# Kernel optimization log

Measured on AMD Instinct MI355X. Metric: run time of the kernel, lower is better.

Reference implementation:

```python
import jax, jax.numpy as jnp
import numpy as np

N_NODES = 100000
N_EDGES = 3200000
D_IN = 128
D_HID = 128
D_FF = 256
N_CLASSES = 26
N_GRAPHS = 512


def setup_inputs() -> dict:
    key = jax.random.key(0)
    ks = jax.random.split(key, 12)
    s = 0.05
    return {
        "x": jax.random.normal(ks[0], (N_NODES, D_IN), dtype=jnp.float32),
        "edge_index": jax.random.randint(ks[1], (2, N_EDGES), 0, N_NODES, dtype=jnp.int64),
        "batch": jnp.sort(jax.random.randint(ks[2], (N_NODES,), 0, N_GRAPHS, dtype=jnp.int64)),
        "W1": jax.random.normal(ks[3], (D_IN, D_HID), dtype=jnp.float32) * s,
        "b1": jnp.zeros((D_HID,), dtype=jnp.float32),
        "W2": jax.random.normal(ks[4], (D_HID, D_HID), dtype=jnp.float32) * s,
        "b2": jnp.zeros((D_HID,), dtype=jnp.float32),
        "W3": jax.random.normal(ks[5], (D_HID, D_HID), dtype=jnp.float32) * s,
        "b3": jnp.zeros((D_HID,), dtype=jnp.float32),
        "Wfc": jax.random.normal(ks[6], (D_HID, D_FF), dtype=jnp.float32) * s,
        "bfc": jnp.zeros((D_FF,), dtype=jnp.float32),
        "Wfc2": jax.random.normal(ks[7], (D_FF, N_CLASSES), dtype=jnp.float32) * s,
        "bfc2": jnp.zeros((N_CLASSES,), dtype=jnp.float32),
    }


def _gcn_layer(x, src, dst, norm, W, b):
    # GCNConv: h = x @ W; out[dst] += norm_e * h[src]; out += b
    h = x @ W                                   # [N, D]
    msg = h[src] * norm[:, None]                # [E+N, D] gather + scale
    agg = jax.ops.segment_sum(msg, dst, num_segments=N_NODES)
    return agg + b


def reference(x, edge_index, batch, W1, b1, W2, b2, W3, b3, Wfc, bfc, Wfc2, bfc2):
    # add self-loops (PyG GCNConv default) and compute symmetric normalization once
    loop = jnp.arange(N_NODES, dtype=edge_index.dtype)
    src = jnp.concatenate([edge_index[0], loop])
    dst = jnp.concatenate([edge_index[1], loop])
    deg = jax.ops.segment_sum(jnp.ones_like(dst, dtype=x.dtype), dst, num_segments=N_NODES)
    dinv = jnp.where(deg > 0, jax.lax.rsqrt(deg), 0.0)
    norm = dinv[src] * dinv[dst]               # D^{-1/2} A_hat D^{-1/2}

    h = jax.nn.relu(_gcn_layer(x, src, dst, norm, W1, b1))
    h = jax.nn.relu(_gcn_layer(h, src, dst, norm, W2, b2))
    h = jax.nn.relu(_gcn_layer(h, src, dst, norm, W3, b3))

    # global mean pool over graphs
    sums = jax.ops.segment_sum(h, batch, num_segments=N_GRAPHS)       # [G, D]
    cnts = jax.ops.segment_sum(jnp.ones((h.shape[0],), h.dtype), batch, num_segments=N_GRAPHS)
    pooled = sums / jnp.maximum(cnts, 1.0)[:, None]

    out = jax.nn.relu(pooled @ Wfc + bfc)       # dropout is identity at inference
    return out @ Wfc2 + bfc2                    # [G, num_classes]
```

## Files before the change

### kernel.cpp

```cpp
#include <hip/hip_runtime.h>
#include <hip/hip_bf16.h>

typedef __bf16 bf16;
typedef __attribute__((ext_vector_type(8))) __bf16 bf16x8;
typedef __attribute__((ext_vector_type(4))) float f32x4;

constexpr int N_NODES   = 100000;
constexpr int N_PAD     = 100032;
constexpr int D         = 128;
constexpr int D_FF      = 256;
constexpr int N_CLASSES = 26;
constexpr int N_GRAPHS  = 512;
constexpr int NB1       = 256;
constexpr int NBUCK     = (N_NODES + 511) / 512;

__device__ inline float2 bf2f(unsigned u) {
    float lo = __uint_as_float(u << 16);
    float hi = __uint_as_float(u & 0xffff0000u);
    return make_float2(lo, hi);
}


__global__ __launch_bounds__(1024) void p1_hist(const int* __restrict__ edst,
                                                int* __restrict__ gcount, int e) {
    __shared__ int cnt[NBUCK];
    for (int t = threadIdx.x; t < NBUCK; t += 1024) cnt[t] = 0;
    __syncthreads();
    int chunk = (e + NB1 - 1) / NB1;
    int lo = blockIdx.x * chunk;
    int hi = min(e, lo + chunk);
    for (int i = lo + threadIdx.x; i < hi; i += 1024)
        atomicAdd(&cnt[edst[i] >> 9], 1);
    __syncthreads();
    for (int t = threadIdx.x; t < NBUCK; t += 1024)
        gcount[t * NB1 + blockIdx.x] = cnt[t];
}

__global__ __launch_bounds__(256) void scan1(const int* __restrict__ in,
                                             int* out, int* bsum, int n) {
    __shared__ int sd[256];
    int i = blockIdx.x * 256 + threadIdx.x;
    int v = (i < n) ? in[i] : 0;
    sd[threadIdx.x] = v; __syncthreads();
    for (int off = 1; off < 256; off <<= 1) {
        int t = (threadIdx.x >= off) ? sd[threadIdx.x - off] : 0;
        __syncthreads();
        sd[threadIdx.x] += t;
        __syncthreads();
    }
    if (i < n) out[i] = sd[threadIdx.x] - v;
    if (threadIdx.x == 255) bsum[blockIdx.x] = sd[255];
}

__global__ __launch_bounds__(1024) void misc_kernel(const int* __restrict__ bsum,
                                                    int* __restrict__ boff, int nb,
                                                    const int* __restrict__ batch,
                                                    int* __restrict__ starts, int n,
                                                    const float* __restrict__ W0,
                                                    const float* __restrict__ W1,
                                                    const float* __restrict__ W2,
                                                    bf16* __restrict__ WT3) {
    int t = threadIdx.x;
    if (blockIdx.x == 0) {
        if (t <= N_GRAPHS) {
            int lo = 0, hi = n;
            while (lo < hi) {
                int mid = (lo + hi) >> 1;
                if (batch[mid] < t) lo = mid + 1; else hi = mid;
            }
            starts[t] = lo;
        }
        __shared__ int sd[1024];
        int v = (t < nb) ? bsum[t] : 0;
        sd[t] = v; __syncthreads();
        for (int off = 1; off < 1024; off <<= 1) {
            int x = (t >= off) ? sd[t - off] : 0;
            __syncthreads();
            sd[t] += x;
            __syncthreads();
        }
        if (t < nb) boff[t] = sd[t] - v;
    } else {
        int idx = (blockIdx.x - 1) * 1024 + t;
        int l = idx >> 14;
        int rem = idx & 16383;
        int nn = rem >> 7;
        int kk = rem & 127;
        const float* W = (l == 0) ? W0 : (l == 1) ? W1 : W2;
        WT3[idx] = (bf16)W[kk * D + nn];
    }
}

__global__ __launch_bounds__(1024) void p3_scatter(const int* __restrict__ esrc,
                                                   const int* __restrict__ edst,
                                                   const int* __restrict__ gbase,
                                                   const int* __restrict__ boff,
                                                   int* __restrict__ ebuf, int e) {
    __shared__ int cur[NBUCK];
    for (int t = threadIdx.x; t < NBUCK; t += 1024)
        cur[t] = gbase[t * NB1 + blockIdx.x] + boff[t];
    __syncthreads();
    int chunk = (e + NB1 - 1) / NB1;
    int lo = blockIdx.x * chunk;
    int hi = min(e, lo + chunk);
    for (int i = lo + threadIdx.x; i < hi; i += 1024) {
        int d = edst[i], s = esrc[i];
        int pos = atomicAdd(&cur[d >> 9], 1);
        ebuf[pos] = (s << 9) | (d & 511);
    }
}

__global__ __launch_bounds__(1024) void p45_fill(const int* __restrict__ ebuf,
                                                 const int* __restrict__ gbase,
                                                 const int* __restrict__ boff,
                                                 float* __restrict__ dinv,
                                                 int* __restrict__ rowptr,
                                                 int* __restrict__ csrc, int e, int n) {
    __shared__ int cnt[512];
    __shared__ int ps[512];
    __shared__ int cur[512];
    int b = blockIdx.x, t = threadIdx.x;
    if (t < 512) cnt[t] = 0;
    __syncthreads();
    int lo = gbase[b * NB1] + boff[b];
    int hi = (b + 1 < NBUCK) ? gbase[(b + 1) * NB1] + boff[b + 1] : e;
    for (int i = lo + t; i < hi; i += 1024)
        atomicAdd(&cnt[ebuf[i] & 511], 1);
    __syncthreads();
    int a = (t < 512) ? cnt[t] : 0;
    if (t < 512) ps[t] = a;
    __syncthreads();
    for (int off = 1; off < 512; off <<= 1) {
        int v = (t >= off && t < 512) ? ps[t - off] : 0;
        __syncthreads();
        if (t < 512) ps[t] += v;
        __syncthreads();
    }
    if (t < 512) {
        int g0 = lo + ps[t] - a;
        int node = b * 512 + t;
        cur[t] = g0;
        if (node < n) {
            rowptr[node] = g0;
            dinv[node] = 1.0f / sqrtf((float)(a + 1));
        }
    }
    if (b == 0 && t == 0) rowptr[n] = e;
    __syncthreads();
    for (int i = lo + t; i < hi; i += 1024) {
        int pe = ebuf[i];
        int pos = atomicAdd(&cur[pe & 511], 1);
        csrc[pos] = pe >> 9;
    }
}


__global__ __launch_bounds__(256) void gemm_f32_kernel(const float* __restrict__ A,
                                                       const bf16* __restrict__ WT,
                                                       bf16* __restrict__ C,
                                                       const float* __restrict__ dinv, int n) {
    int wave = threadIdx.x >> 6;
    int lane = threadIdx.x & 63;
    int m16  = lane & 15;
    int quad = lane >> 4;
    int row0 = blockIdx.x * 64 + wave * 16;
    int arowi = row0 + m16;

    bf16x8 a[4];
    const float* arow = A + (size_t)arowi * D + quad * 8;
#pragma unroll
    for (int kt = 0; kt < 4; ++kt) {
        float4 f0 = make_float4(0.f, 0.f, 0.f, 0.f);
        float4 f1 = make_float4(0.f, 0.f, 0.f, 0.f);
        if (arowi < n) {
            f0 = *(const float4*)(arow + kt * 32);
            f1 = *(const float4*)(arow + kt * 32 + 4);
        }
        bf16x8 v = { (bf16)f0.x, (bf16)f0.y, (bf16)f0.z, (bf16)f0.w,
                     (bf16)f1.x, (bf16)f1.y, (bf16)f1.z, (bf16)f1.w };
        a[kt] = v;
    }

    float sc[4];
#pragma unroll
    for (int r = 0; r < 4; ++r) {
        int rr = row0 + quad * 4 + r;
        sc[r] = (rr < n) ? dinv[rr] : 0.f;
    }

#pragma unroll
    for (int nt = 0; nt < 8; ++nt) {
        f32x4 acc = {0.f, 0.f, 0.f, 0.f};
        const bf16* brow = WT + (nt * 16 + m16) * D + quad * 8;
#pragma unroll
        for (int kt = 0; kt < 4; ++kt) {
            bf16x8 b = *(const bf16x8*)(brow + kt * 32);
            acc = __builtin_amdgcn_mfma_f32_16x16x32_bf16(a[kt], b, acc, 0, 0, 0);
        }
#pragma unroll
        for (int r = 0; r < 4; ++r)
            C[(row0 + quad * 4 + r) * D + nt * 16 + m16] = (bf16)(sc[r] * acc[r]);
    }
}

__device__ inline void agg_node(const bf16* __restrict__ h, int v, int n, int c,
                                const int* __restrict__ rowptr,
                                const int* __restrict__ csrc,
                                const float* __restrict__ dinv,
                                float& dv, float acc[8]) {
    int s = 0, e = 0;
    dv = 0.f;
    if (v < n) { s = rowptr[v]; e = rowptr[v + 1]; dv = dinv[v]; }
#pragma unroll
    for (int d = 0; d < 8; ++d) acc[d] = 0.f;
    if (v < n) {
        uint4 u = *(const uint4*)(h + (size_t)v * D + c * 8);
        float2 f0 = bf2f(u.x), f1 = bf2f(u.y), f2 = bf2f(u.z), f3 = bf2f(u.w);
        acc[0] = f0.x; acc[1] = f0.y; acc[2] = f1.x; acc[3] = f1.y;
        acc[4] = f2.x; acc[5] = f2.y; acc[6] = f3.x; acc[7] = f3.y;
    }
    int j = s;
    for (; j + 3 < e; j += 4) {
        int s0 = csrc[j], s1 = csrc[j + 1], s2 = csrc[j + 2], s3 = csrc[j + 3];
        uint4 u0 = *(const uint4*)(h + (size_t)s0 * D + c * 8);
        uint4 u1 = *(const uint4*)(h + (size_t)s1 * D + c * 8);
        uint4 u2 = *(const uint4*)(h + (size_t)s2 * D + c * 8);
        uint4 u3 = *(const uint4*)(h + (size_t)s3 * D + c * 8);
        {
            float2 a0 = bf2f(u0.x), a1 = bf2f(u0.y), a2 = bf2f(u0.z), a3 = bf2f(u0.w);
            acc[0] += a0.x; acc[1] += a0.y; acc[2] += a1.x; acc[3] += a1.y;
            acc[4] += a2.x; acc[5] += a2.y; acc[6] += a3.x; acc[7] += a3.y;
        }
        {
            float2 a0 = bf2f(u1.x), a1 = bf2f(u1.y), a2 = bf2f(u1.z), a3 = bf2f(u1.w);
            acc[0] += a0.x; acc[1] += a0.y; acc[2] += a1.x; acc[3] += a1.y;
            acc[4] += a2.x; acc[5] += a2.y; acc[6] += a3.x; acc[7] += a3.y;
        }
        {
            float2 a0 = bf2f(u2.x), a1 = bf2f(u2.y), a2 = bf2f(u2.z), a3 = bf2f(u2.w);
            acc[0] += a0.x; acc[1] += a0.y; acc[2] += a1.x; acc[3] += a1.y;
            acc[4] += a2.x; acc[5] += a2.y; acc[6] += a3.x; acc[7] += a3.y;
        }
        {
            float2 a0 = bf2f(u3.x), a1 = bf2f(u3.y), a2 = bf2f(u3.z), a3 = bf2f(u3.w);
            acc[0] += a0.x; acc[1] += a0.y; acc[2] += a1.x; acc[3] += a1.y;
            acc[4] += a2.x; acc[5] += a2.y; acc[6] += a3.x; acc[7] += a3.y;
        }
    }
    for (; j < e; ++j) {
        int s0 = csrc[j];
        uint4 u0 = *(const uint4*)(h + (size_t)s0 * D + c * 8);
        float2 a0 = bf2f(u0.x), a1 = bf2f(u0.y), a2 = bf2f(u0.z), a3 = bf2f(u0.w);
        acc[0] += a0.x; acc[1] += a0.y; acc[2] += a1.x; acc[3] += a1.y;
        acc[4] += a2.x; acc[5] += a2.y; acc[6] += a3.x; acc[7] += a3.y;
    }
}

__device__ inline bf16x8 relu_row(float dv, const float acc[8],
                                  const float* __restrict__ bias, int c) {
    float4 bi0 = *(const float4*)(bias + c * 8);
    float4 bi1 = *(const float4*)(bias + c * 8 + 4);
    bf16x8 o;
    o[0] = (bf16)fmaxf(fmaf(dv, acc[0], bi0.x), 0.f);
    o[1] = (bf16)fmaxf(fmaf(dv, acc[1], bi0.y), 0.f);
    o[2] = (bf16)fmaxf(fmaf(dv, acc[2], bi0.z), 0.f);
    o[3] = (bf16)fmaxf(fmaf(dv, acc[3], bi0.w), 0.f);
    o[4] = (bf16)fmaxf(fmaf(dv, acc[4], bi1.x), 0.f);
    o[5] = (bf16)fmaxf(fmaf(dv, acc[5], bi1.y), 0.f);
    o[6] = (bf16)fmaxf(fmaf(dv, acc[6], bi1.z), 0.f);
    o[7] = (bf16)fmaxf(fmaf(dv, acc[7], bi1.w), 0.f);
    return o;
}

__global__ __launch_bounds__(256) void spmm_gemm_kernel(const bf16* __restrict__ h,
                                                        const int* __restrict__ rowptr,
                                                        const int* __restrict__ csrc,
                                                        const float* __restrict__ dinv,
                                                        const float* __restrict__ bias,
                                                        const bf16* __restrict__ WT,
                                                        bf16* __restrict__ C, int n) {
    __shared__ bf16 tile[16][136];
    int t = threadIdx.x;
    int grp = t >> 4;
    int c   = t & 15;
    int v   = blockIdx.x * 16 + grp;
    float dv, acc[8];
    agg_node(h, v, n, c, rowptr, csrc, dinv, dv, acc);
    *(bf16x8*)(&tile[grp][c * 8]) = relu_row(dv, acc, bias, c);
    __syncthreads();

    int wave = t >> 6, lane = t & 63;
    int m16 = lane & 15, quad = lane >> 4;
    bf16x8 a[4];
#pragma unroll
    for (int kt = 0; kt < 4; ++kt)
        a[kt] = *(const bf16x8*)(&tile[m16][quad * 8 + kt * 32]);

    int base = blockIdx.x * 16;
    float sc[4];
#pragma unroll
    for (int r = 0; r < 4; ++r) {
        int rr = base + quad * 4 + r;
        sc[r] = (rr < n) ? dinv[rr] : 0.f;
    }

#pragma unroll
    for (int nt2 = 0; nt2 < 2; ++nt2) {
        int nt = wave * 2 + nt2;
        f32x4 accq = {0.f, 0.f, 0.f, 0.f};
        const bf16* brow = WT + (nt * 16 + m16) * D + quad * 8;
#pragma unroll
        for (int kt = 0; kt < 4; ++kt) {
            bf16x8 b = *(const bf16x8*)(brow + kt * 32);
            accq = __builtin_amdgcn_mfma_f32_16x16x32_bf16(a[kt], b, accq, 0, 0, 0);
        }
#pragma unroll
        for (int r = 0; r < 4; ++r)
            C[(size_t)(base + quad * 4 + r) * D + nt * 16 + m16] = (bf16)(sc[r] * accq[r]);
    }
}

__global__ __launch_bounds__(256) void spmm2_kernel(const bf16* __restrict__ h,
                                                    const int* __restrict__ rowptr,
                                                    const int* __restrict__ csrc,
                                                    const float* __restrict__ dinv,
                                                    const float* __restrict__ bias,
                                                    bf16* __restrict__ out, int n) {
    int t = threadIdx.x;
    int grp = t >> 4;
    int c   = t & 15;
    int v   = blockIdx.x * 16 + grp;
    float dv, acc[8];
    agg_node(h, v, n, c, rowptr, csrc, dinv, dv, acc);
    if (v < n)
        *(bf16x8*)(out + (size_t)v * D + c * 8) = relu_row(dv, acc, bias, c);
}

__global__ __launch_bounds__(256) void poolfc_kernel(const bf16* __restrict__ h,
                                                     const int* __restrict__ starts,
                                                     const float* __restrict__ Wfc,
                                                     const float* __restrict__ bfc,
                                                     const float* __restrict__ Wfc2,
                                                     const float* __restrict__ bfc2,
                                                     float* __restrict__ out) {
    __shared__ float part[3][D];
    __shared__ float pr[D];
    __shared__ float hid[D_FF];
    __shared__ float red[N_CLASSES][9];
    int g = blockIdx.x;
    int w = threadIdx.x >> 6, lane = threadIdx.x & 63;
    int s = starts[g], e = starts[g + 1];
    float ax = 0.f, ay = 0.f;
    for (int r = s + w; r < e; r += 4) {
        unsigned u = *(const unsigned*)(h + r * D + lane * 2);
        float2 f = bf2f(u);
        ax += f.x; ay += f.y;
    }
    if (w > 0) { part[w - 1][lane * 2] = ax; part[w - 1][lane * 2 + 1] = ay; }
    __syncthreads();
    if (w == 0) {
#pragma unroll
        for (int k = 0; k < 3; ++k) { ax += part[k][lane * 2]; ay += part[k][lane * 2 + 1]; }
        float c = fmaxf((float)(e - s), 1.0f);
        pr[lane * 2]     = ax / c;
        pr[lane * 2 + 1] = ay / c;
    }
    __syncthreads();
    int t = threadIdx.x;
    float a0 = 0.f, a1 = 0.f, a2 = 0.f, a3 = 0.f;
    for (int k = 0; k < D; k += 4) {
        a0 = fmaf(pr[k],     Wfc[k * D_FF + t],       a0);
        a1 = fmaf(pr[k + 1], Wfc[(k + 1) * D_FF + t], a1);
        a2 = fmaf(pr[k + 2], Wfc[(k + 2) * D_FF + t], a2);
        a3 = fmaf(pr[k + 3], Wfc[(k + 3) * D_FF + t], a3);
    }
    hid[t] = fmaxf((a0 + a1) + (a2 + a3) + bfc[t], 0.f);
    __syncthreads();
    if (t < N_CLASSES * 8) {
        int cls = t >> 3, kk = t & 7;
        float o = 0.f;
        for (int k = kk; k < D_FF; k += 8)
            o = fmaf(hid[k], Wfc2[k * N_CLASSES + cls], o);
        red[cls][kk] = o;
    }
    __syncthreads();
    if (t < N_CLASSES) {
        float o = bfc2[t];
#pragma unroll
        for (int k = 0; k < 8; ++k) o += red[t][k];
        out[g * N_CLASSES + t] = o;
    }
}


extern "C" void kernel_launch(void* const* d_in, const int* in_sizes, int n_in,
                              void* d_out, int out_size, void* d_ws, size_t ws_size,
                              hipStream_t stream) {
    const float* x     = (const float*)d_in[0];
    const int*   eidx  = (const int*)d_in[1];
    const int*   batch = (const int*)d_in[2];
    const float* W[3]  = { (const float*)d_in[3], (const float*)d_in[5], (const float*)d_in[7] };
    const float* b[3]  = { (const float*)d_in[4], (const float*)d_in[6], (const float*)d_in[8] };
    const float* Wfc   = (const float*)d_in[9];
    const float* bfc   = (const float*)d_in[10];
    const float* Wfc2  = (const float*)d_in[11];
    const float* bfc2  = (const float*)d_in[12];
    float* out = (float*)d_out;

    const int E = in_sizes[1] / 2;
    const int N = in_sizes[0] / D;
    const int* esrc = eidx;
    const int* edst = eidx + E;

    uint8_t* base = (uint8_t*)d_ws;
    size_t off = 0;
    auto alloc = [&](size_t bytes) -> void* {
        void* p = base + off;
        off = (off + bytes + 255) & ~(size_t)255;
        return p;
    };
    bf16*  hA     = (bf16*) alloc((size_t)N_PAD * D * 2);
    bf16*  hB     = (bf16*) alloc((size_t)N_PAD * D * 2);
    bf16*  WT3    = (bf16*) alloc((size_t)3 * D * D * 2);
    int*   csrc   = (int*)  alloc((size_t)E * 4);
    int*   ebuf   = (int*)  alloc((size_t)E * 4);
    int*   gcount = (int*)  alloc((size_t)NBUCK * NB1 * 4);
    int*   gbase  = (int*)  alloc((size_t)(NBUCK * NB1 + 1) * 4);
    int*   rowptr = (int*)  alloc((size_t)(N + 1) * 4);
    float* dinv   = (float*)alloc((size_t)N * 4);
    int*   bsum   = (int*)  alloc(4096);
    int*   boff   = (int*)  alloc(4096);
    int*   starts = (int*)  alloc((size_t)(N_GRAPHS + 1) * 4);
    (void)ws_size; (void)n_in; (void)out_size;

    const int GB  = N_PAD / 64;
    const int SGB = N_PAD / 16;
    const int GCN = NBUCK * NB1;
    const int GCB = (GCN + 255) / 256;

    p1_hist<<<NB1, 1024, 0, stream>>>(edst, gcount, E);
    scan1<<<GCB, 256, 0, stream>>>(gcount, gbase, bsum, GCN);
    misc_kernel<<<49, 1024, 0, stream>>>(bsum, boff, GCB, batch, starts, N,
                                         W[0], W[1], W[2], WT3);
    p3_scatter<<<NB1, 1024, 0, stream>>>(esrc, edst, gbase, boff, ebuf, E);
    p45_fill<<<NBUCK, 1024, 0, stream>>>(ebuf, gbase, boff, dinv, rowptr, csrc, E, N);

    gemm_f32_kernel<<<GB, 256, 0, stream>>>(x, WT3, hA, dinv, N);
    spmm_gemm_kernel<<<SGB, 256, 0, stream>>>(hA, rowptr, csrc, dinv, b[0],
                                              WT3 + (size_t)1 * D * D, hB, N);
    spmm_gemm_kernel<<<SGB, 256, 0, stream>>>(hB, rowptr, csrc, dinv, b[1],
                                              WT3 + (size_t)2 * D * D, hA, N);
    spmm2_kernel<<<SGB, 256, 0, stream>>>(hA, rowptr, csrc, dinv, b[2], hB, N);

    poolfc_kernel<<<N_GRAPHS, 256, 0, stream>>>(hB, starts, Wfc, bfc, Wfc2, bfc2, out);
}
```

Measured before the change: 580.6 us.

## Fuse mean-pool into last aggregation and add nontemporal loads/stores

The final SpMM no longer writes the layer-3 activations. It reduces each 16-node tile per graph in shared memory and atomically adds the result into a zeroed per-graph float sum buffer, and the FC head then only divides by node counts. This removes the write of the node activations and the separate pooling pass that read them back. Separately, the GEMM input loads, the CSR index loads and the bf16 output stores are made nontemporal to reduce cache pollution. The fused path adds float atomics, which makes summation order nondeterministic.

After: 617.6 us. +6.4%, slower.

```diff
diff --git a/kernel.cpp b/kernel.cpp
--- a/kernel.cpp
+++ b/kernel.cpp
@@ -18,6 +18,12 @@
     float lo = __uint_as_float(u << 16);
     float hi = __uint_as_float(u & 0xffff0000u);
     return make_float2(lo, hi);
+}
+
+__device__ inline void nt_store_bf16(bf16* p, float f) {
+    bf16 v = (bf16)f;
+    short s = *reinterpret_cast<short*>(&v);
+    __builtin_nontemporal_store(s, reinterpret_cast<short*>(p));
 }
 
 
@@ -59,7 +65,8 @@
                                                     const float* __restrict__ W0,
                                                     const float* __restrict__ W1,
                                                     const float* __restrict__ W2,
-                                                    bf16* __restrict__ WT3) {
+                                                    bf16* __restrict__ WT3,
+                                                    float* __restrict__ gsum) {
     int t = threadIdx.x;
     if (blockIdx.x == 0) {
         if (t <= N_GRAPHS) {
@@ -80,7 +87,7 @@
             __syncthreads();
         }
         if (t < nb) boff[t] = sd[t] - v;
-    } else {
+    } else if (blockIdx.x <= 48) {
         int idx = (blockIdx.x - 1) * 1024 + t;
         int l = idx >> 14;
         int rem = idx & 16383;
@@ -88,6 +95,10 @@
         int kk = rem & 127;
         const float* W = (l == 0) ? W0 : (l == 1) ? W1 : W2;
         WT3[idx] = (bf16)W[kk * D + nn];
+    } else {
+        int idx = (blockIdx.x - 49) * 1024 + t;
+        f32x4 z = {0.f, 0.f, 0.f, 0.f};
+        *((f32x4*)gsum + idx) = z;
     }
 }
 
@@ -170,14 +181,14 @@
     const float* arow = A + (size_t)arowi * D + quad * 8;
 #pragma unroll
     for (int kt = 0; kt < 4; ++kt) {
-        float4 f0 = make_float4(0.f, 0.f, 0.f, 0.f);
-        float4 f1 = make_float4(0.f, 0.f, 0.f, 0.f);
+        f32x4 f0 = {0.f, 0.f, 0.f, 0.f};
+        f32x4 f1 = {0.f, 0.f, 0.f, 0.f};
         if (arowi < n) {
-            f0 = *(const float4*)(arow + kt * 32);
-            f1 = *(const float4*)(arow + kt * 32 + 4);
-        }
-        bf16x8 v = { (bf16)f0.x, (bf16)f0.y, (bf16)f0.z, (bf16)f0.w,
-                     (bf16)f1.x, (bf16)f1.y, (bf16)f1.z, (bf16)f1.w };
+            f0 = __builtin_nontemporal_load((const f32x4*)(arow + kt * 32));
+            f1 = __builtin_nontemporal_load((const f32x4*)(arow + kt * 32 + 4));
+        }
+        bf16x8 v = { (bf16)f0[0], (bf16)f0[1], (bf16)f0[2], (bf16)f0[3],
+                     (bf16)f1[0], (bf16)f1[1], (bf16)f1[2], (bf16)f1[3] };
         a[kt] = v;
     }
 
@@ -199,7 +210,7 @@
         }
 #pragma unroll
         for (int r = 0; r < 4; ++r)
-            C[(row0 + quad * 4 + r) * D + nt * 16 + m16] = (bf16)(sc[r] * acc[r]);
+            nt_store_bf16(&C[(row0 + quad * 4 + r) * D + nt * 16 + m16], sc[r] * acc[r]);
     }
 }
 
@@ -221,7 +232,10 @@
     }
     int j = s;
     for (; j + 3 < e; j += 4) {
-        int s0 = csrc[j], s1 = csrc[j + 1], s2 = csrc[j + 2], s3 = csrc[j + 3];
+        int s0 = __builtin_nontemporal_load(csrc + j);
+        int s1 = __builtin_nontemporal_load(csrc + j + 1);
+        int s2 = __builtin_nontemporal_load(csrc + j + 2);
+        int s3 = __builtin_nontemporal_load(csrc + j + 3);
         uint4 u0 = *(const uint4*)(h + (size_t)s0 * D + c * 8);
         uint4 u1 = *(const uint4*)(h + (size_t)s1 * D + c * 8);
         uint4 u2 = *(const uint4*)(h + (size_t)s2 * D + c * 8);
@@ -248,28 +262,12 @@
         }
     }
     for (; j < e; ++j) {
-        int s0 = csrc[j];
+        int s0 = __builtin_nontemporal_load(csrc + j);
         uint4 u0 = *(const uint4*)(h + (size_t)s0 * D + c * 8);
         float2 a0 = bf2f(u0.x), a1 = bf2f(u0.y), a2 = bf2f(u0.z), a3 = bf2f(u0.w);
         acc[0] += a0.x; acc[1] += a0.y; acc[2] += a1.x; acc[3] += a1.y;
         acc[4] += a2.x; acc[5] += a2.y; acc[6] += a3.x; acc[7] += a3.y;
     }
-}
-
-__device__ inline bf16x8 relu_row(float dv, const float acc[8],
-                                  const float* __restrict__ bias, int c) {
-    float4 bi0 = *(const float4*)(bias + c * 8);
-    float4 bi1 = *(const float4*)(bias + c * 8 + 4);
-    bf16x8 o;
-    o[0] = (bf16)fmaxf(fmaf(dv, acc[0], bi0.x), 0.f);
-    o[1] = (bf16)fmaxf(fmaf(dv, acc[1], bi0.y), 0.f);
-    o[2] = (bf16)fmaxf(fmaf(dv, acc[2], bi0.z), 0.f);
-    o[3] = (bf16)fmaxf(fmaf(dv, acc[3], bi0.w), 0.f);
-    o[4] = (bf16)fmaxf(fmaf(dv, acc[4], bi1.x), 0.f);
-    o[5] = (bf16)fmaxf(fmaf(dv, acc[5], bi1.y), 0.f);
-    o[6] = (bf16)fmaxf(fmaf(dv, acc[6], bi1.z), 0.f);
-    o[7] = (bf16)fmaxf(fmaf(dv, acc[7], bi1.w), 0.f);
-    return o;
 }
 
 __global__ __launch_bounds__(256) void spmm_gemm_kernel(const bf16* __restrict__ h,
@@ -286,7 +284,20 @@
     int v   = blockIdx.x * 16 + grp;
     float dv, acc[8];
     agg_node(h, v, n, c, rowptr, csrc, dinv, dv, acc);
-    *(bf16x8*)(&tile[grp][c * 8]) = relu_row(dv, acc, bias, c);
+    {
+        float4 bi0 = *(const float4*)(bias + c * 8);
+        float4 bi1 = *(const float4*)(bias + c * 8 + 4);
+        bf16x8 o;
+        o[0] = (bf16)fmaxf(fmaf(dv, acc[0], bi0.x), 0.f);
+        o[1] = (bf16)fmaxf(fmaf(dv, acc[1], bi0.y), 0.f);
+        o[2] = (bf16)fmaxf(fmaf(dv, acc[2], bi0.z), 0.f);
+        o[3] = (bf16)fmaxf(fmaf(dv, acc[3], bi0.w), 0.f);
+        o[4] = (bf16)fmaxf(fmaf(dv, acc[4], bi1.x), 0.f);
+        o[5] = (bf16)fmaxf(fmaf(dv, acc[5], bi1.y), 0.f);
+        o[6] = (bf16)fmaxf(fmaf(dv, acc[6], bi1.z), 0.f);
+        o[7] = (bf16)fmaxf(fmaf(dv, acc[7], bi1.w), 0.f);
+        *(bf16x8*)(&tile[grp][c * 8]) = o;
+    }
     __syncthreads();
 
     int wave = t >> 6, lane = t & 63;
@@ -316,57 +327,78 @@
         }
 #pragma unroll
         for (int r = 0; r < 4; ++r)
-            C[(size_t)(base + quad * 4 + r) * D + nt * 16 + m16] = (bf16)(sc[r] * accq[r]);
-    }
-}
-
-__global__ __launch_bounds__(256) void spmm2_kernel(const bf16* __restrict__ h,
-                                                    const int* __restrict__ rowptr,
-                                                    const int* __restrict__ csrc,
-                                                    const float* __restrict__ dinv,
-                                                    const float* __restrict__ bias,
-                                                    bf16* __restrict__ out, int n) {
+            nt_store_bf16(&C[(size_t)(base + quad * 4 + r) * D + nt * 16 + m16],
+                          sc[r] * accq[r]);
+    }
+}
+
+__global__ __launch_bounds__(256) void spmm2_pool_kernel(const bf16* __restrict__ h,
+                                                         const int* __restrict__ rowptr,
+                                                         const int* __restrict__ csrc,
+                                                         const float* __restrict__ dinv,
+                                                         const float* __restrict__ bias,
+                                                         const int* __restrict__ batch,
+                                                         float* __restrict__ gsum, int n) {
+    __shared__ float tile[16][D];
+    __shared__ int gid[16];
     int t = threadIdx.x;
     int grp = t >> 4;
     int c   = t & 15;
     int v   = blockIdx.x * 16 + grp;
     float dv, acc[8];
     agg_node(h, v, n, c, rowptr, csrc, dinv, dv, acc);
-    if (v < n)
-        *(bf16x8*)(out + (size_t)v * D + c * 8) = relu_row(dv, acc, bias, c);
-}
-
-__global__ __launch_bounds__(256) void poolfc_kernel(const bf16* __restrict__ h,
-                                                     const int* __restrict__ starts,
-                                                     const float* __restrict__ Wfc,
-                                                     const float* __restrict__ bfc,
-                                                     const float* __restrict__ Wfc2,
-                                                     const float* __restrict__ bfc2,
-                                                     float* __restrict__ out) {
-    __shared__ float part[3][D];
+    float4 bi0 = *(const float4*)(bias + c * 8);
+    float4 bi1 = *(const float4*)(bias + c * 8 + 4);
+    float r0 = fmaxf(fmaf(dv, acc[0], bi0.x), 0.f);
+    float r1 = fmaxf(fmaf(dv, acc[1], bi0.y), 0.f);
+    float r2 = fmaxf(fmaf(dv, acc[2], bi0.z), 0.f);
+    float r3 = fmaxf(fmaf(dv, acc[3], bi0.w), 0.f);
+    float r4 = fmaxf(fmaf(dv, acc[4], bi1.x), 0.f);
+    float r5 = fmaxf(fmaf(dv, acc[5], bi1.y), 0.f);
+    float r6 = fmaxf(fmaf(dv, acc[6], bi1.z), 0.f);
+    float r7 = fmaxf(fmaf(dv, acc[7], bi1.w), 0.f);
+    if (v >= n) { r0 = r1 = r2 = r3 = r4 = r5 = r6 = r7 = 0.f; }
+    tile[grp][c * 8 + 0] = r0; tile[grp][c * 8 + 1] = r1;
+    tile[grp][c * 8 + 2] = r2; tile[grp][c * 8 + 3] = r3;
+    tile[grp][c * 8 + 4] = r4; tile[grp][c * 8 + 5] = r5;
+    tile[grp][c * 8 + 6] = r6; tile[grp][c * 8 + 7] = r7;
+    if (c == 0) gid[grp] = (v < n) ? batch[v] : -1;
+    __syncthreads();
+    if (t < D) {
+        int curg = gid[0];
+        float sum = 0.f;
+        if (curg >= 0) {
+#pragma unroll 1
+            for (int k = 0; k < 16; ++k) {
+                int gg = gid[k];
+                if (gg < 0) break;
+                if (gg != curg) {
+                    atomicAdd(&gsum[(size_t)curg * D + t], sum);
+                    curg = gg; sum = 0.f;
+                }
+                sum += tile[k][t];
+            }
+            atomicAdd(&gsum[(size_t)curg * D + t], sum);
+        }
+    }
+}
+
+__global__ __launch_bounds__(256) void fc_head_kernel(const float* __restrict__ gsum,
+                                                      const int* __restrict__ starts,
+                                                      const float* __restrict__ Wfc,
+                                                      const float* __restrict__ bfc,
+                                                      const float* __restrict__ Wfc2,
+                                                      const float* __restrict__ bfc2,
+                                                      float* __restrict__ out) {
     __shared__ float pr[D];
     __shared__ float hid[D_FF];
     __shared__ float red[N_CLASSES][9];
-    int g = blockIdx.x;
-    int w = threadIdx.x >> 6, lane = threadIdx.x & 63;
-    int s = starts[g], e = starts[g + 1];
-    float ax = 0.f, ay = 0.f;
-    for (int r = s + w; r < e; r += 4) {
-        unsigned u = *(const unsigned*)(h + r * D + lane * 2);
-        float2 f = bf2f(u);
-        ax += f.x; ay += f.y;
-    }
-    if (w > 0) { part[w - 1][lane * 2] = ax; part[w - 1][lane * 2 + 1] = ay; }
-    __syncthreads();
-    if (w == 0) {
-#pragma unroll
-        for (int k = 0; k < 3; ++k) { ax += part[k][lane * 2]; ay += part[k][lane * 2 + 1]; }
-        float c = fmaxf((float)(e - s), 1.0f);
-        pr[lane * 2]     = ax / c;
-        pr[lane * 2 + 1] = ay / c;
-    }
-    __syncthreads();
-    int t = threadIdx.x;
+    int g = blockIdx.x, t = threadIdx.x;
+    if (t < D) {
+        float ccount = fmaxf((float)(starts[g + 1] - starts[g]), 1.0f);
+        pr[t] = gsum[(size_t)g * D + t] / ccount;
+    }
+    __syncthreads();
     float a0 = 0.f, a1 = 0.f, a2 = 0.f, a3 = 0.f;
     for (int k = 0; k < D; k += 4) {
         a0 = fmaf(pr[k],     Wfc[k * D_FF + t],       a0);
@@ -431,17 +463,18 @@
     int*   bsum   = (int*)  alloc(4096);
     int*   boff   = (int*)  alloc(4096);
     int*   starts = (int*)  alloc((size_t)(N_GRAPHS + 1) * 4);
+    float* gsum   = (float*)alloc((size_t)N_GRAPHS * D * 4);
     (void)ws_size; (void)n_in; (void)out_size;
 
     const int GB  = N_PAD / 64;
-    const int SGB = N_PAD / 16;
+    const int SGB = (N + 15) / 16;
     const int GCN = NBUCK * NB1;
     const int GCB = (GCN + 255) / 256;
 
     p1_hist<<<NB1, 1024, 0, stream>>>(edst, gcount, E);
     scan1<<<GCB, 256, 0, stream>>>(gcount, gbase, bsum, GCN);
-    misc_kernel<<<49, 1024, 0, stream>>>(bsum, boff, GCB, batch, starts, N,
-                                         W[0], W[1], W[2], WT3);
+    misc_kernel<<<65, 1024, 0, stream>>>(bsum, boff, GCB, batch, starts, N,
+                                         W[0], W[1], W[2], WT3, gsum);
     p3_scatter<<<NB1, 1024, 0, stream>>>(esrc, edst, gbase, boff, ebuf, E);
     p45_fill<<<NBUCK, 1024, 0, stream>>>(ebuf, gbase, boff, dinv, rowptr, csrc, E, N);
 
@@ -450,7 +483,8 @@
                                               WT3 + (size_t)1 * D * D, hB, N);
     spmm_gemm_kernel<<<SGB, 256, 0, stream>>>(hB, rowptr, csrc, dinv, b[1],
                                               WT3 + (size_t)2 * D * D, hA, N);
-    spmm2_kernel<<<SGB, 256, 0, stream>>>(hA, rowptr, csrc, dinv, b[2], hB, N);
-
-    poolfc_kernel<<<N_GRAPHS, 256, 0, stream>>>(hB, starts, Wfc, bfc, Wfc2, bfc2, out);
-}
+    spmm2_pool_kernel<<<SGB, 256, 0, stream>>>(hA, rowptr, csrc, dinv, b[2],
+                                               batch, gsum, N);
+
+    fc_head_kernel<<<N_GRAPHS, 256, 0, stream>>>(gsum, starts, Wfc, bfc, Wfc2, bfc2, out);
+}
```
